# Performance work log

Measured on AMD Instinct MI355X. Metric: run time of the kernel, lower is better.

The kernel has to match this reference:

```python
import jax, jax.numpy as jnp
import numpy as np
import math

B, T, D = 1, 2048, 2048
H, HD = 16, 128          # n_head, head_dim = D // H
L = 512                  # latent_dims
RD = 64                  # rope_dims
K = 32                   # top-k selected tokens per query
THETA = 10000.0


def rope_tables(rd, t_max):
    freqs = 1.0 / (THETA ** (jnp.arange(0, rd, 2, dtype=jnp.float32) / rd))
    t = jnp.arange(t_max, dtype=jnp.float32)
    ang = jnp.outer(t, freqs)                      # (T, rd/2)
    cos = jnp.concatenate([jnp.cos(ang), jnp.cos(ang)], axis=-1)  # (T, rd)
    sin = jnp.concatenate([jnp.sin(ang), jnp.sin(ang)], axis=-1)
    return cos, sin


def rotate_half(x):
    d = x.shape[-1] // 2
    return jnp.concatenate([-x[..., d:], x[..., :d]], axis=-1)


def apply_rope(x, cos, sin):
    # x: (B, H, T, rd); cos/sin: (T, rd) -> broadcast over B, H
    t = x.shape[2]
    return x * cos[None, None, :t] + rotate_half(x) * sin[None, None, :t]


def setup_inputs() -> dict:
    key = jax.random.key(0)
    ks = jax.random.split(key, 10)
    s = lambda fan_in: 1.0 / math.sqrt(fan_in)
    inp = {
        'x': jax.random.normal(ks[0], (B, T, D), dtype=jnp.float32),
        'Wqd': jax.random.normal(ks[1], (D, L), dtype=jnp.float32) * s(D),
        'Wqu': jax.random.normal(ks[2], (L, D), dtype=jnp.float32) * s(L),
        'Wqr': jax.random.normal(ks[3], (L, H * RD), dtype=jnp.float32) * s(L),
        'Wkvd': jax.random.normal(ks[4], (D, L), dtype=jnp.float32) * s(D),
        'Wku': jax.random.normal(ks[5], (L, D), dtype=jnp.float32) * s(L),
        'Wvu': jax.random.normal(ks[6], (L, D), dtype=jnp.float32) * s(L),
        'Wkr': jax.random.normal(ks[7], (D, RD), dtype=jnp.float32) * s(D),
        'Wo': jax.random.normal(ks[8], (D, D), dtype=jnp.float32) * s(D),
        'topk_idx': jax.random.randint(ks[9], (B, T, K), 0, T, dtype=jnp.int64)
            if jax.config.jax_enable_x64 else
            jax.random.randint(ks[9], (B, T, K), 0, T, dtype=jnp.int32),
    }
    return inp


def reference(x, Wqd, Wqu, Wqr, Wkvd, Wku, Wvu, Wkr, Wo, topk_idx):
    cos, sin = rope_tables(RD, T)

    ql = x @ Wqd                                               # (B,T,L)
    q = (ql @ Wqu).reshape(B, T, H, HD).transpose(0, 2, 1, 3)  # (B,H,T,hd)
    qr = (ql @ Wqr).reshape(B, T, H, RD).transpose(0, 2, 1, 3)
    qr = apply_rope(qr, cos, sin)                              # (B,H,T,rd)

    ckv = x @ Wkvd                                             # (B,T,L)
    k = (ckv @ Wku).reshape(B, T, H, HD).transpose(0, 2, 1, 3) # (B,H,T,hd)
    v = (ckv @ Wvu).reshape(B, T, H, HD).transpose(0, 2, 1, 3)
    kr = apply_rope((x @ Wkr)[:, None], cos, sin)[:, 0]        # (B,T,rd) shared across heads

    # top-k gather sparse attention path
    flat = topk_idx.reshape(B, T * K)                          # (B, T*K)
    k_sel = jax.vmap(lambda a, i: a[:, i])(k, flat).reshape(B, H, T, K, HD)
    v_sel = jax.vmap(lambda a, i: a[:, i])(v, flat).reshape(B, H, T, K, HD)
    kr_sel = jax.vmap(lambda a, i: a[i])(kr, flat).reshape(B, T, K, RD)

    scale = 1.0 / math.sqrt(HD + RD)
    scores = (jnp.einsum('bhtd,bhtkd->bhtk', q, k_sel)
              + jnp.einsum('bhtd,btkd->bhtk', qr, kr_sel)) * scale
    attn = jax.nn.softmax(scores, axis=-1)                     # (B,H,T,K)
    out = jnp.einsum('bhtk,bhtkd->bhtd', attn, v_sel)          # (B,H,T,hd)
    out = out.transpose(0, 2, 1, 3).reshape(B, T, D)
    return out @ Wo
```

## Files before the change

### kernel.cpp

```cpp
#include <hip/hip_runtime.h>
#include <hip/hip_bf16.h>
#include <math.h>

typedef __hip_bfloat16 bf16;
typedef __attribute__((ext_vector_type(4))) float f32x4;
typedef __attribute__((ext_vector_type(8))) short s16x8;

#define T_SEQ 2048
#define DIM   2048
#define NH    16
#define LAT   512
#define RD    64
#define TOPK  32

typedef const __attribute__((address_space(1))) void* gas_ptr;
typedef __attribute__((address_space(3))) void* las_ptr;

struct GGroup {
    const bf16* A; const bf16* BT; bf16* C;
    int K, lda, ldb, ldc;
    int tx, ty, nz;
    long aZ, bZ, cZ;
    int tiles;
    int flags, N, t0;
};
struct GPack { GGroup g[4]; int n; };

__global__ __launch_bounds__(256)
void gemm128(GPack gp)
{
    int b = blockIdx.x;
    int gi = 0;
    while (gi < gp.n - 1 && b >= gp.g[gi].tiles) { b -= gp.g[gi].tiles; ++gi; }
    const GGroup g = gp.g[gi];

    {
        const int nwg = g.tiles;
        const int xcd = b & 7, idx = b >> 3;
        const int qq = nwg >> 3, rr = nwg & 7;
        b = (xcd < rr ? xcd * (qq + 1) : rr * (qq + 1) + (xcd - rr) * qq) + idx;
    }

    const int per_z = g.tx * g.ty;
    const int z   = b / per_z;
    const int rem = b - z * per_z;
    const int bx  = rem % g.tx;
    const int by  = rem / g.tx;

    const bf16* A  = g.A  + (size_t)z * g.aZ;
    const bf16* BT = g.BT + (size_t)z * g.bZ;
    bf16*       C  = g.C  + (size_t)z * g.cZ;

    __shared__ bf16 aL[128 * 64];
    __shared__ bf16 bL[128 * 64];

    const int tid  = threadIdx.x;
    const int wave = tid >> 6;
    const int lane = tid & 63;
    const int quad = lane >> 4;
    const int l16  = lane & 15;

    const int tile_m = by * 128;
    const int tile_n = bx * 128;
    const int wm = (wave >> 1) * 64;
    const int wn = (wave & 1) * 64;

    const int lrow = lane >> 3;
    const int lke  = (((lane & 7) ^ lrow) * 8);
    const int sw   = l16 & 7;

    f32x4 acc[4][4] = {};

    for (int k0 = 0; k0 < g.K; k0 += 64) {
#pragma unroll
        for (int p = 0; p < 4; ++p) {
            const int R = (wave * 4 + p) * 8;
            const bf16* srcA = A + (size_t)(tile_m + R + lrow) * g.lda + k0 + lke;
            __builtin_amdgcn_global_load_lds((gas_ptr)srcA, (las_ptr)(aL + R * 64), 16, 0, 0);
            int brow = tile_n + R + lrow;
            if (g.flags & 2) brow = brow < g.N ? brow : g.N - 1;
            const bf16* srcB = BT + (size_t)brow * g.ldb + k0 + lke;
            __builtin_amdgcn_global_load_lds((gas_ptr)srcB, (las_ptr)(bL + R * 64), 16, 0, 0);
        }
        __syncthreads();

#pragma unroll
        for (int ks = 0; ks < 2; ++ks) {
            const int seg = ((ks * 4 + quad) ^ sw) * 8;
            s16x8 af[4], bf_[4];
#pragma unroll
            for (int i = 0; i < 4; ++i)
                af[i] = *(const s16x8*)(&aL[(wm + i * 16 + l16) * 64 + seg]);
#pragma unroll
            for (int j = 0; j < 4; ++j)
                bf_[j] = *(const s16x8*)(&bL[(wn + j * 16 + l16) * 64 + seg]);

#pragma unroll
            for (int i = 0; i < 4; ++i)
#pragma unroll
                for (int j = 0; j < 4; ++j)
                    acc[i][j] = __builtin_amdgcn_mfma_f32_16x16x32_bf16(
                        af[i], bf_[j], acc[i][j], 0, 0, 0);
        }
        __syncthreads();
    }

    if (g.flags & 1) {
#pragma unroll
        for (int jp = 0; jp < 2; ++jp) {
            const int colL = tile_n + wn + jp * 16 + l16;
            if ((g.flags & 2) && colL >= g.N) continue;
            const float fr = powf(10000.f, -(float)(jp * 16 + l16) / 32.f);
#pragma unroll
            for (int i = 0; i < 4; ++i) {
#pragma unroll
                for (int r = 0; r < 4; ++r) {
                    const int row = tile_m + wm + i * 16 + quad * 4 + r;
                    float sv, cv;
                    sincosf((float)(g.t0 + row) * fr, &sv, &cv);
                    const float x0 = acc[i][jp][r];
                    const float x1 = acc[i][jp + 2][r];
                    C[(size_t)row * g.ldc + colL]      = __float2bfloat16(x0 * cv - x1 * sv);
                    C[(size_t)row * g.ldc + colL + 32] = __float2bfloat16(x1 * cv + x0 * sv);
                }
            }
        }
    } else if (g.flags & 4) {
        float* Cf = (float*)C;
#pragma unroll
        for (int j = 0; j < 4; ++j) {
            const int col = tile_n + wn + j * 16 + l16;
#pragma unroll
            for (int i = 0; i < 4; ++i)
#pragma unroll
                for (int r = 0; r < 4; ++r) {
                    const int row = tile_m + wm + i * 16 + quad * 4 + r;
                    Cf[(size_t)row * g.ldc + col] = acc[i][j][r];
                }
        }
    } else {
#pragma unroll
        for (int j = 0; j < 4; ++j) {
            const int col = tile_n + wn + j * 16 + l16;
            if ((g.flags & 2) && col >= g.N) continue;
#pragma unroll
            for (int i = 0; i < 4; ++i)
#pragma unroll
                for (int r = 0; r < 4; ++r) {
                    const int row = tile_m + wm + i * 16 + quad * 4 + r;
                    C[(size_t)row * g.ldc + col] = __float2bfloat16(acc[i][j][r]);
                }
        }
    }
}

struct TDesc { const float* src; bf16* dst; int R; int C; int tiles; int ctiles; };
struct TPack { TDesc d[8]; int n; };

__global__ __launch_bounds__(256)
void transpose_batch(TPack p)
{
    int b = blockIdx.x;
    int mi = 0;
    while (mi < p.n - 1 && b >= p.d[mi].tiles) { b -= p.d[mi].tiles; ++mi; }
    const TDesc d = p.d[mi];
    const int tr = b / d.ctiles, tc = b % d.ctiles;
    const int r0 = tr * 32, c0 = tc * 32;

    __shared__ float lds[32][33];
    const int tx = threadIdx.x & 31, ty = threadIdx.x >> 5;
#pragma unroll
    for (int i = 0; i < 4; ++i)
        lds[ty * 4 + i][tx] = d.src[(size_t)(r0 + ty * 4 + i) * d.C + c0 + tx];
    __syncthreads();
#pragma unroll
    for (int i = 0; i < 4; ++i)
        d.dst[(size_t)(c0 + ty * 4 + i) * d.R + r0 + tx] =
            __float2bfloat16(lds[tx][ty * 4 + i]);
}

__global__ __launch_bounds__(256)
void convert2(const float* s0, bf16* d0, int n0,
              const float* s1, bf16* d1, int n1)
{
    int i = blockIdx.x * blockDim.x + threadIdx.x;
    const float* s; bf16* d;
    if (i < n0) { s = s0; d = d0; }
    else if (i < n0 + n1) { i -= n0; s = s1; d = d1; }
    else return;
    const float4 a = *(const float4*)(s + (size_t)i * 8);
    const float4 b = *(const float4*)(s + (size_t)i * 8 + 4);
    bf16 t[8];
    t[0] = __float2bfloat16(a.x); t[1] = __float2bfloat16(a.y);
    t[2] = __float2bfloat16(a.z); t[3] = __float2bfloat16(a.w);
    t[4] = __float2bfloat16(b.x); t[5] = __float2bfloat16(b.y);
    t[6] = __float2bfloat16(b.z); t[7] = __float2bfloat16(b.w);
    *(uint4*)(d + (size_t)i * 8) = *(uint4*)t;
}

__global__ __launch_bounds__(256)
void attn_mla(const bf16* __restrict__ qt,
              const bf16* __restrict__ qr,
              const bf16* __restrict__ xw,
              const bf16* __restrict__ kr,
              const int*  __restrict__ topk,
              bf16* __restrict__ U,
              int t0)
{
    __shared__ short ckv_s[32 * 520];
    __shared__ short kr_s[32 * 72];
    __shared__ short qr_s[16 * 72];
    __shared__ short P_s[4][16 * 40];
    __shared__ int   idx_s[32];

    const int tl   = blockIdx.x;
    const int tg   = t0 + tl;
    const int tid  = threadIdx.x;
    const int wv   = tid >> 6;
    const int lane = tid & 63;
    const int quad = lane >> 4;
    const int l16  = lane & 15;

    if (tid < 32) {
        int j = topk[(size_t)tg * TOPK + tid];
        idx_s[tid] = (j < 0 || j >= T_SEQ) ? 0 : j;
    }
    __syncthreads();

#pragma unroll
    for (int i = 0; i < 8; ++i) {
        const int row = wv * 8 + i;
        const int j = idx_s[row];
        __builtin_amdgcn_global_load_lds(
            (gas_ptr)(xw + (size_t)j * 1024 + 512 + lane * 8),
            (las_ptr)(ckv_s + row * 520), 16, 0, 0);
    }
    {
        const int row = tid >> 3, seg = tid & 7;
        const int j = idx_s[row];
        *(uint4*)(kr_s + row * 72 + seg * 8) =
            *(const uint4*)(kr + (size_t)j * RD + seg * 8);
    }
    if (tid < 128) {
        const int head = tid >> 3, seg = tid & 7;
        *(uint4*)(qr_s + head * 72 + seg * 8) =
            *(const uint4*)(qr + (size_t)tl * 1024 + head * 64 + seg * 8);
    }
    __syncthreads();

    const bf16* qrow = qt + (size_t)tl * 8192 + l16 * 512;
    f32x4 sc[2] = {};
#pragma unroll
    for (int ks = 0; ks < 16; ++ks) {
        s16x8 a  = *(const s16x8*)(qrow + ks * 32 + quad * 8);
        s16x8 b0 = *(const s16x8*)(ckv_s + l16 * 520 + ks * 32 + quad * 8);
        s16x8 b1 = *(const s16x8*)(ckv_s + (16 + l16) * 520 + ks * 32 + quad * 8);
        sc[0] = __builtin_amdgcn_mfma_f32_16x16x32_bf16(a, b0, sc[0], 0, 0, 0);
        sc[1] = __builtin_amdgcn_mfma_f32_16x16x32_bf16(a, b1, sc[1], 0, 0, 0);
    }
#pragma unroll
    for (int ks = 0; ks < 2; ++ks) {
        s16x8 a  = *(const s16x8*)(qr_s + l16 * 72 + ks * 32 + quad * 8);
        s16x8 b0 = *(const s16x8*)(kr_s + l16 * 72 + ks * 32 + quad * 8);
        s16x8 b1 = *(const s16x8*)(kr_s + (16 + l16) * 72 + ks * 32 + quad * 8);
        sc[0] = __builtin_amdgcn_mfma_f32_16x16x32_bf16(a, b0, sc[0], 0, 0, 0);
        sc[1] = __builtin_amdgcn_mfma_f32_16x16x32_bf16(a, b1, sc[1], 0, 0, 0);
    }

    const float scale = 0.0721687836487032f;
    float inv[4];
    short* pw = P_s[wv];
#pragma unroll
    for (int r = 0; r < 4; ++r) {
        float s0 = sc[0][r] * scale, s1 = sc[1][r] * scale;
        float mx = fmaxf(s0, s1);
#pragma unroll
        for (int off = 1; off < 16; off <<= 1) mx = fmaxf(mx, __shfl_xor(mx, off));
        float p0 = __expf(s0 - mx), p1 = __expf(s1 - mx);
        float l = p0 + p1;
#pragma unroll
        for (int off = 1; off < 16; off <<= 1) l += __shfl_xor(l, off);
        inv[r] = 1.f / l;
        pw[(quad * 4 + r) * 40 + l16]      = __builtin_bit_cast(short, __float2bfloat16(p0));
        pw[(quad * 4 + r) * 40 + 16 + l16] = __builtin_bit_cast(short, __float2bfloat16(p1));
    }

    s16x8 ap = *(const s16x8*)(pw + l16 * 40 + quad * 8);
#pragma unroll
    for (int tt = 0; tt < 8; ++tt) {
        const int n0 = wv * 128 + tt * 16;
        s16x8 b;
#pragma unroll
        for (int j = 0; j < 8; ++j)
            b[j] = ckv_s[(quad * 8 + j) * 520 + n0 + l16];
        f32x4 u = {};
        u = __builtin_amdgcn_mfma_f32_16x16x32_bf16(ap, b, u, 0, 0, 0);
#pragma unroll
        for (int r = 0; r < 4; ++r)
            U[(size_t)tl * 8192 + (quad * 4 + r) * 512 + n0 + l16] =
                __float2bfloat16(u[r] * inv[r]);
    }
}

extern "C" void kernel_launch(void* const* d_in, const int* in_sizes, int n_in,
                              void* d_out, int out_size, void* d_ws, size_t ws_size,
                              hipStream_t stream)
{
    const float* x    = (const float*)d_in[0];
    const float* Wqd  = (const float*)d_in[1];
    const float* Wqu  = (const float*)d_in[2];
    const float* Wqr  = (const float*)d_in[3];
    const float* Wkvd = (const float*)d_in[4];
    const float* Wku  = (const float*)d_in[5];
    const float* Wvu  = (const float*)d_in[6];
    const float* Wkr  = (const float*)d_in[7];
    const float* Wo   = (const float*)d_in[8];
    const int*   topk = (const int*)d_in[9];
    float* out = (float*)d_out;

    const size_t KB = 1024;
    char* ws = (char*)d_ws;
    const bool flat = ws_size >= (size_t)128000 * KB;
    const int  TCH  = flat ? 2048 : 512;
    const int  NCH  = T_SEQ / TCH;

    size_t oXB, oWxT, oWkrT, oWquT, oWkub, oWqrT, oWvuT, oQ, oXW, oKR,
           oQR, oO, oWoT, oQT, oU;
    if (flat) {
        oXB = 0;       oWxT = 8192;   oWkrT = 12288; oWquT = 12544;
        oWkub = 14592; oWqrT = 16640; oWvuT = 17664; oQ = 19712;
        oXW = 27904;   oKR = 32000;   oQR = 32256;   oO = 36352;
        oWoT = 44544;  oQT = 52736;   oU = 85504;
    } else {
        oXW = 0;       oKR = 4096;    oWquT = 4352;  oWkub = 6400;
        oWqrT = 8448;  oWvuT = 9472;  oO = 11520;    oXB = 19712;
        oWxT = 27904;  oWkrT = 32000; oQ = 19712;    oQT = 21760;
        oQR = 29952;   oU = 30976;    oWoT = 21760;
    }
    bf16* xb   = (bf16*)(ws + oXB * KB);
    bf16* WxT  = (bf16*)(ws + oWxT * KB);
    bf16* WkrT = (bf16*)(ws + oWkrT * KB);
    bf16* WquT = (bf16*)(ws + oWquT * KB);
    bf16* Wkub = (bf16*)(ws + oWkub * KB);
    bf16* WqrT = (bf16*)(ws + oWqrT * KB);
    bf16* WvuT = (bf16*)(ws + oWvuT * KB);
    bf16* qB   = (bf16*)(ws + oQ * KB);
    bf16* xw   = (bf16*)(ws + oXW * KB);
    bf16* kr   = (bf16*)(ws + oKR * KB);
    bf16* qrC  = (bf16*)(ws + oQR * KB);
    bf16* o    = (bf16*)(ws + oO * KB);
    bf16* WoT  = (bf16*)(ws + oWoT * KB);
    bf16* qtC  = (bf16*)(ws + oQT * KB);
    bf16* uC   = (bf16*)(ws + oU * KB);

    dim3 blk(256);

    {
        int n0 = T_SEQ * DIM / 8, n1 = LAT * DIM / 8;
        convert2<<<(n0 + n1 + 255) / 256, blk, 0, stream>>>(x, xb, n0, Wku, Wkub, n1);
        TPack p;
        p.d[0] = { Wqd,  WxT,                   DIM, LAT,  (DIM/32)*(LAT/32),  LAT/32 };
        p.d[1] = { Wkvd, WxT + (size_t)LAT*DIM, DIM, LAT,  (DIM/32)*(LAT/32),  LAT/32 };
        p.d[2] = { Wkr,  WkrT,                  DIM, RD,   (DIM/32)*(RD/32),   RD/32  };
        p.d[3] = { Wqr,  WqrT,                  LAT, 1024, (LAT/32)*(1024/32), 1024/32 };
        p.d[4] = { Wvu,  WvuT,                  LAT, DIM,  (LAT/32)*(DIM/32),  DIM/32 };
        p.d[5] = { Wqu,  WquT,                  LAT, DIM,  (LAT/32)*(DIM/32),  DIM/32 };
        p.n = 6;
        int tot = 0;
        for (int i = 0; i < p.n; ++i) tot += p.d[i].tiles;
        if (flat) {
            p.d[6] = { Wo, WoT, DIM, DIM, (DIM/32)*(DIM/32), DIM/32 };
            p.n = 7; tot += p.d[6].tiles;
        }
        transpose_batch<<<tot, blk, 0, stream>>>(p);
    }

    {
        GPack gp;
        gp.g[0] = { xb, WxT,  xw, DIM, DIM, DIM, 1024, 1024/128, T_SEQ/128, 1,
                    0, 0, 0, (1024/128)*(T_SEQ/128), 0, 1024, 0 };
        gp.g[1] = { xb, WkrT, kr, DIM, DIM, DIM, RD,   1,        T_SEQ/128, 1,
                    0, 0, 0, T_SEQ/128, 3 , RD, 0 };
        gp.n = 2;
        gemm128<<<gp.g[0].tiles + gp.g[1].tiles, blk, 0, stream>>>(gp);
    }

    for (int c = 0; c < NCH; ++c) {
        const int t0 = c * TCH;
        bf16* q  = flat ? qB  + (size_t)t0 * 2048 : qB;
        bf16* qt = flat ? qtC + (size_t)t0 * 8192 : qtC;
        bf16* qr = flat ? qrC + (size_t)t0 * 1024 : qrC;
        bf16* U  = flat ? uC  + (size_t)t0 * 8192 : uC;
        const bf16* xwc = xw + (size_t)t0 * 1024;

        {
            GPack gp;
            gp.g[0] = { xwc, WquT, q,  LAT, 1024, LAT, 2048, 2048/128, TCH/128, 1,
                        0, 0, 0, (2048/128)*(TCH/128), 0, 2048, 0 };
            gp.g[1] = { xwc, WqrT, qr, LAT, 1024, LAT, 1024, 1024/128, TCH/128, 1,
                        0, 0, 0, (1024/128)*(TCH/128), 1 , 1024, t0 };
            gp.n = 2;
            gemm128<<<gp.g[0].tiles + gp.g[1].tiles, blk, 0, stream>>>(gp);
        }
        {
            GPack gp;
            gp.g[0] = { q, Wkub, qt, 128, 2048, 2048, 8192, 512/128, TCH/128, NH,
                        128, 128, 512, (512/128)*(TCH/128)*NH, 0, 512, 0 };
            gp.n = 1;
            gemm128<<<gp.g[0].tiles, blk, 0, stream>>>(gp);
        }
        attn_mla<<<TCH, blk, 0, stream>>>(qt, qr, xw, kr, topk, U, t0);
        {
            GPack gp;
            gp.g[0] = { U, WvuT, o + (size_t)t0 * DIM, LAT, 8192, LAT, DIM,
                        1, TCH/128, NH, 512, (long)128*LAT, 128,
                        (TCH/128)*NH, 0, 128, 0 };
            gp.n = 1;
            gemm128<<<gp.g[0].tiles, blk, 0, stream>>>(gp);
        }
    }

    if (!flat) {
        TPack p;
        p.d[0] = { Wo, WoT, DIM, DIM, (DIM/32)*(DIM/32), DIM/32 };
        p.n = 1;
        transpose_batch<<<p.d[0].tiles, blk, 0, stream>>>(p);
    }
    {
        GPack gp;
        gp.g[0] = { o, WoT, (bf16*)out, DIM, DIM, DIM, DIM,
                    DIM/128, T_SEQ/128, 1, 0, 0, 0,
                    (DIM/128)*(T_SEQ/128), 4 , DIM, 0 };
        gp.n = 1;
        gemm128<<<gp.g[0].tiles, blk, 0, stream>>>(gp);
    }
}
```

Measured before the change: 277.0 us.

## Use 64x64-tile GEMM for latent projection and split attention score K across waves

```diff
diff --git a/kernel.cpp b/kernel.cpp
--- a/kernel.cpp
+++ b/kernel.cpp
@@ -25,6 +25,139 @@
     int flags, N, t0;
 };
 struct GPack { GGroup g[4]; int n; };
+
+template<int MT>
+__global__ __launch_bounds__(256)
+void gemm_group(GPack gp)
+{
+    constexpr int MI = MT / 64;
+
+    int b = blockIdx.x;
+    int gi = 0;
+    while (gi < gp.n - 1 && b >= gp.g[gi].tiles) { b -= gp.g[gi].tiles; ++gi; }
+    const GGroup g = gp.g[gi];
+
+    {
+        const int nwg = g.tiles;
+        const int xcd = b & 7, idx = b >> 3;
+        const int qq = nwg >> 3, rr = nwg & 7;
+        b = (xcd < rr ? xcd * (qq + 1) : rr * (qq + 1) + (xcd - rr) * qq) + idx;
+    }
+
+    const int per_z = g.tx * g.ty;
+    const int z   = b / per_z;
+    const int rem = b - z * per_z;
+    const int bx  = rem % g.tx;
+    const int by  = rem / g.tx;
+
+    const bf16* A  = g.A  + (size_t)z * g.aZ;
+    const bf16* BT = g.BT + (size_t)z * g.bZ;
+    bf16*       C  = g.C  + (size_t)z * g.cZ;
+
+    __shared__ bf16 aL[MT * 64];
+    __shared__ bf16 bL[64 * 64];
+
+    const int tid  = threadIdx.x;
+    const int wave = tid >> 6;
+    const int lane = tid & 63;
+    const int quad = lane >> 4;
+    const int l16  = lane & 15;
+
+    const int tile_m = by * MT;
+    const int tile_n = bx * 64;
+    const int wrow = wave * (MT / 4);
+
+    const int lrow = lane >> 3;
+    const int lke  = (((lane & 7) ^ lrow) * 8);
+    const int sw   = l16 & 7;
+
+    f32x4 acc[MI][4] = {};
+
+    for (int k0 = 0; k0 < g.K; k0 += 64) {
+#pragma unroll
+        for (int p = 0; p < 2 * MI; ++p) {
+            const int R = (wave * 2 * MI + p) * 8;
+            const bf16* src = A + (size_t)(tile_m + R + lrow) * g.lda + k0 + lke;
+            __builtin_amdgcn_global_load_lds((gas_ptr)src, (las_ptr)(aL + R * 64), 16, 0, 0);
+        }
+#pragma unroll
+        for (int p = 0; p < 2; ++p) {
+            const int R = (wave * 2 + p) * 8;
+            const bf16* src = BT + (size_t)(tile_n + R + lrow) * g.ldb + k0 + lke;
+            __builtin_amdgcn_global_load_lds((gas_ptr)src, (las_ptr)(bL + R * 64), 16, 0, 0);
+        }
+        __syncthreads();
+
+#pragma unroll
+        for (int ks = 0; ks < 2; ++ks) {
+            s16x8 af[MI], bfr[4];
+#pragma unroll
+            for (int i = 0; i < MI; ++i)
+                af[i] = *(const s16x8*)(&aL[(wrow + i * 16 + l16) * 64 +
+                                            (((ks * 4 + quad) ^ sw) * 8)]);
+#pragma unroll
+            for (int j = 0; j < 4; ++j)
+                bfr[j] = *(const s16x8*)(&bL[(j * 16 + l16) * 64 +
+                                             (((ks * 4 + quad) ^ sw) * 8)]);
+
+#pragma unroll
+            for (int i = 0; i < MI; ++i)
+#pragma unroll
+                for (int j = 0; j < 4; ++j)
+                    acc[i][j] = __builtin_amdgcn_mfma_f32_16x16x32_bf16(
+                        af[i], bfr[j], acc[i][j], 0, 0, 0);
+        }
+        __syncthreads();
+    }
+
+    if (g.flags & 1) {
+#pragma unroll
+        for (int jp = 0; jp < 2; ++jp) {
+            const int colL = tile_n + jp * 16 + l16;
+            if ((g.flags & 2) && colL >= g.N) continue;
+            const float fr = powf(10000.f, -(float)(jp * 16 + l16) / 32.f);
+#pragma unroll
+            for (int i = 0; i < MI; ++i) {
+#pragma unroll
+                for (int r = 0; r < 4; ++r) {
+                    const int row = tile_m + wrow + i * 16 + quad * 4 + r;
+                    float sv, cv;
+                    sincosf((float)(g.t0 + row) * fr, &sv, &cv);
+                    const float x0 = acc[i][jp][r];
+                    const float x1 = acc[i][jp + 2][r];
+                    C[(size_t)row * g.ldc + colL]      = __float2bfloat16(x0 * cv - x1 * sv);
+                    C[(size_t)row * g.ldc + colL + 32] = __float2bfloat16(x1 * cv + x0 * sv);
+                }
+            }
+        }
+    } else if (g.flags & 4) {
+        float* Cf = (float*)C;
+#pragma unroll
+        for (int j = 0; j < 4; ++j) {
+            const int col = tile_n + j * 16 + l16;
+#pragma unroll
+            for (int i = 0; i < MI; ++i)
+#pragma unroll
+                for (int r = 0; r < 4; ++r) {
+                    const int row = tile_m + wrow + i * 16 + quad * 4 + r;
+                    Cf[(size_t)row * g.ldc + col] = acc[i][j][r];
+                }
+        }
+    } else {
+#pragma unroll
+        for (int j = 0; j < 4; ++j) {
+            const int col = tile_n + j * 16 + l16;
+            if ((g.flags & 2) && col >= g.N) continue;
+#pragma unroll
+            for (int i = 0; i < MI; ++i)
+#pragma unroll
+                for (int r = 0; r < 4; ++r) {
+                    const int row = tile_m + wrow + i * 16 + quad * 4 + r;
+                    C[(size_t)row * g.ldc + col] = __float2bfloat16(acc[i][j][r]);
+                }
+        }
+    }
+}
 
 __global__ __launch_bounds__(256)
 void gemm128(GPack gp)
@@ -211,6 +344,7 @@
     __shared__ short kr_s[32 * 72];
     __shared__ short qr_s[16 * 72];
     __shared__ short P_s[4][16 * 40];
+    __shared__ float red[4][64][4];
     __shared__ int   idx_s[32];
 
     const int tl   = blockIdx.x;
@@ -251,21 +385,32 @@
     const bf16* qrow = qt + (size_t)tl * 8192 + l16 * 512;
     f32x4 sc[2] = {};
 #pragma unroll
-    for (int ks = 0; ks < 16; ++ks) {
+    for (int kk = 0; kk < 4; ++kk) {
+        const int ks = wv * 4 + kk;
         s16x8 a  = *(const s16x8*)(qrow + ks * 32 + quad * 8);
         s16x8 b0 = *(const s16x8*)(ckv_s + l16 * 520 + ks * 32 + quad * 8);
         s16x8 b1 = *(const s16x8*)(ckv_s + (16 + l16) * 520 + ks * 32 + quad * 8);
         sc[0] = __builtin_amdgcn_mfma_f32_16x16x32_bf16(a, b0, sc[0], 0, 0, 0);
         sc[1] = __builtin_amdgcn_mfma_f32_16x16x32_bf16(a, b1, sc[1], 0, 0, 0);
     }
-#pragma unroll
-    for (int ks = 0; ks < 2; ++ks) {
+    if (wv < 2) {
+        const int ks = wv;
         s16x8 a  = *(const s16x8*)(qr_s + l16 * 72 + ks * 32 + quad * 8);
         s16x8 b0 = *(const s16x8*)(kr_s + l16 * 72 + ks * 32 + quad * 8);
         s16x8 b1 = *(const s16x8*)(kr_s + (16 + l16) * 72 + ks * 32 + quad * 8);
         sc[0] = __builtin_amdgcn_mfma_f32_16x16x32_bf16(a, b0, sc[0], 0, 0, 0);
         sc[1] = __builtin_amdgcn_mfma_f32_16x16x32_bf16(a, b1, sc[1], 0, 0, 0);
     }
+
+    *(f32x4*)red[wv][lane] = sc[0];
+    __syncthreads();
+    sc[0] = *(const f32x4*)red[0][lane] + *(const f32x4*)red[1][lane] +
+            *(const f32x4*)red[2][lane] + *(const f32x4*)red[3][lane];
+    __syncthreads();
+    *(f32x4*)red[wv][lane] = sc[1];
+    __syncthreads();
+    sc[1] = *(const f32x4*)red[0][lane] + *(const f32x4*)red[1][lane] +
+            *(const f32x4*)red[2][lane] + *(const f32x4*)red[3][lane];
 
     const float scale = 0.0721687836487032f;
     float inv[4];
@@ -377,12 +522,12 @@
 
     {
         GPack gp;
-        gp.g[0] = { xb, WxT,  xw, DIM, DIM, DIM, 1024, 1024/128, T_SEQ/128, 1,
-                    0, 0, 0, (1024/128)*(T_SEQ/128), 0, 1024, 0 };
-        gp.g[1] = { xb, WkrT, kr, DIM, DIM, DIM, RD,   1,        T_SEQ/128, 1,
-                    0, 0, 0, T_SEQ/128, 3 , RD, 0 };
+        gp.g[0] = { xb, WxT,  xw, DIM, DIM, DIM, 1024, 1024/64, T_SEQ/64, 1,
+                    0, 0, 0, (1024/64)*(T_SEQ/64), 0, 1024, 0 };
+        gp.g[1] = { xb, WkrT, kr, DIM, DIM, DIM, RD,   1,       T_SEQ/64, 1,
+                    0, 0, 0, T_SEQ/64, 1 , RD, 0 };
         gp.n = 2;
-        gemm128<<<gp.g[0].tiles + gp.g[1].tiles, blk, 0, stream>>>(gp);
+        gemm_group<64><<<gp.g[0].tiles + gp.g[1].tiles, blk, 0, stream>>>(gp);
     }
 
     for (int c = 0; c < NCH; ++c) {
```

Result: faster. 253.4 us (-8.5%).
